# Performance work log

Measured on AMD Instinct MI355X. Metric: run time of the kernel, lower is better.

The kernel has to match this reference:

```python
import jax, jax.numpy as jnp
import numpy as np

N = 2048   # transform dimensionality n
M = 2048   # number of Householder reflectors m (== n -> full expressiveness)
B = 4096   # batch size
H1 = 1.0   # constant for U[-1,-1] when n == m


def setup_inputs() -> dict:
    key = jax.random.key(0)
    k1, k2 = jax.random.split(key)
    x = jax.random.normal(k1, (B, N), dtype=jnp.float32)
    weight = jax.random.normal(k2, (N, M), dtype=jnp.float32)
    return {"x": x, "weight": weight}


def _apply_reflections(x, weight):
    # U = weight.triu(); U[-1,-1] = h1 since n == m
    U = jnp.triu(weight)
    U = U.at[-1, -1].set(jnp.asarray(H1, weight.dtype))
    h = x.T  # (n, B)

    def step(h, u):
        # h <- h - (2 / ||u||^2) * u (u^T h); skip if u == 0 (matches n2==0 branch)
        n2sq = jnp.dot(u, u)
        safe = jnp.where(n2sq > 0, n2sq, jnp.ones_like(n2sq))
        coef = jnp.where(n2sq > 0, 2.0 / safe, jnp.zeros_like(n2sq))
        proj = u @ h  # (B,)
        return h - coef * u[:, None] * proj[None, :], None

    # forward loop runs i = m-1 .. 0, i.e. over reversed rows of U
    h, _ = jax.lax.scan(step, h, U[::-1])
    return h.T  # (B, n)


def reference(x, weight):
    return _apply_reflections(x, weight)
```

## Files before the change

### kernel.cpp

```cpp
#include <hip/hip_runtime.h>


#define NT 2048
#define NT128 16
#define LSTR 48

typedef __attribute__((ext_vector_type(8))) short bf16x8;
typedef __attribute__((ext_vector_type(4))) float f32x4;
typedef unsigned short ushort_t;

__device__ __forceinline__ ushort_t f2bf_rtne(float f) {
  unsigned u = __builtin_bit_cast(unsigned, f);
  u += 0x7FFFu + ((u >> 16) & 1u);
  return (ushort_t)(u >> 16);
}
__device__ __forceinline__ float bf2f(ushort_t h) {
  return __builtin_bit_cast(float, (unsigned)h << 16);
}


__global__ __launch_bounds__(256)
void prep_zero_kernel(const float* __restrict__ w,
                      ushort_t* __restrict__ UMh, ushort_t* __restrict__ UMl,
                      float* __restrict__ Tz) {
  const int b = blockIdx.x;
  if (b >= 4096) {
    const size_t base = ((size_t)(b - 4096) * 256 + threadIdx.x) * 16;
    const float4 z = make_float4(0.f, 0.f, 0.f, 0.f);
#pragma unroll
    for (int q = 0; q < 4; ++q) *(float4*)(Tz + base + q * 4) = z;
    return;
  }
  const size_t i4 = ((size_t)b * 256 + threadIdx.x) * 4;
  const int j = (int)(i4 >> 11);
  const int c = (int)(i4 & (NT - 1));
  const float4 v = *(const float4*)(w + i4);
  float f[4] = {v.x, v.y, v.z, v.w};
  ushort_t h[4], l[4];
#pragma unroll
  for (int q = 0; q < 4; ++q) {
    const int cc = c + q;
    float val = f[q];
    if (j == NT - 1 && cc == NT - 1) val = 1.0f;
    val = (cc >= j) ? val : 0.f;
    h[q] = f2bf_rtne(val);
    l[q] = f2bf_rtne(val - bf2f(h[q]));
  }
  *(uint2*)(UMh + i4) = make_uint2((unsigned)h[0] | ((unsigned)h[1] << 16),
                                   (unsigned)h[2] | ((unsigned)h[3] << 16));
  *(uint2*)(UMl + i4) = make_uint2((unsigned)l[0] | ((unsigned)l[1] << 16),
                                   (unsigned)l[2] | ((unsigned)l[3] << 16));
}


__device__ __forceinline__ void stage_f32ld(const float* __restrict__ src,
                                            int rb, int kb, int t, int ld,
                                            ushort_t* __restrict__ Hd,
                                            ushort_t* __restrict__ Ld) {
  const int r0 = t >> 3;
  const int seg = (t & 7) * 4;
#pragma unroll
  for (int p = 0; p < 4; ++p) {
    const int row = r0 + p * 32;
    const float4 v = *(const float4*)(src + (size_t)(rb + row) * ld + kb + seg);
    const float f[4] = {v.x, v.y, v.z, v.w};
    ushort_t h[4], l[4];
#pragma unroll
    for (int q = 0; q < 4; ++q) {
      h[q] = f2bf_rtne(f[q]);
      l[q] = f2bf_rtne(f[q] - bf2f(h[q]));
    }
    const int o = row * LSTR + seg;
    *(uint2*)(Hd + o) = make_uint2((unsigned)h[0] | ((unsigned)h[1] << 16),
                                   (unsigned)h[2] | ((unsigned)h[3] << 16));
    *(uint2*)(Ld + o) = make_uint2((unsigned)l[0] | ((unsigned)l[1] << 16),
                                   (unsigned)l[2] | ((unsigned)l[3] << 16));
  }
}

__device__ __forceinline__ void stage_a2(const float* __restrict__ A0,
                                         const float* __restrict__ A1,
                                         int rb, int kb, int t, int ld,
                                         ushort_t* __restrict__ Hd,
                                         ushort_t* __restrict__ Ld) {
  const int r0 = t >> 3;
  const int seg = (t & 7) * 4;
#pragma unroll
  for (int p = 0; p < 4; ++p) {
    const int row = r0 + p * 32;
    const size_t g = (size_t)(rb + row) * ld + kb + seg;
    const float4 v0 = *(const float4*)(A0 + g);
    const float4 v1 = *(const float4*)(A1 + g);
    const float f[4] = {v0.x + v1.x, v0.y + v1.y, v0.z + v1.z, v0.w + v1.w};
    ushort_t h[4], l[4];
#pragma unroll
    for (int q = 0; q < 4; ++q) {
      h[q] = f2bf_rtne(f[q]);
      l[q] = f2bf_rtne(f[q] - bf2f(h[q]));
    }
    const int o = row * LSTR + seg;
    *(uint2*)(Hd + o) = make_uint2((unsigned)h[0] | ((unsigned)h[1] << 16),
                                   (unsigned)h[2] | ((unsigned)h[3] << 16));
    *(uint2*)(Ld + o) = make_uint2((unsigned)l[0] | ((unsigned)l[1] << 16),
                                   (unsigned)l[2] | ((unsigned)l[3] << 16));
  }
}

__device__ __forceinline__ void stage_pre(const ushort_t* __restrict__ H,
                                          const ushort_t* __restrict__ L,
                                          int rb, int kb, int t,
                                          ushort_t* __restrict__ Hd,
                                          ushort_t* __restrict__ Ld) {
  const int r0 = t >> 1;
  const int seg = (t & 1) << 4;
  const size_t g = (size_t)(rb + r0) * NT + kb + seg;
  const int o = r0 * LSTR + seg;
  *(bf16x8*)(Hd + o) = *(const bf16x8*)(H + g);
  *(bf16x8*)(Hd + o + 8) = *(const bf16x8*)(H + g + 8);
  *(bf16x8*)(Ld + o) = *(const bf16x8*)(L + g);
  *(bf16x8*)(Ld + o + 8) = *(const bf16x8*)(L + g + 8);
}

__device__ __forceinline__ void stage_pre1(const ushort_t* __restrict__ H,
                                           int rb, int kb, int t,
                                           ushort_t* __restrict__ Hd) {
  const int r0 = t >> 1;
  const int seg = (t & 1) << 4;
  const size_t g = (size_t)(rb + r0) * NT + kb + seg;
  const int o = r0 * LSTR + seg;
  *(bf16x8*)(Hd + o) = *(const bf16x8*)(H + g);
  *(bf16x8*)(Hd + o + 8) = *(const bf16x8*)(H + g + 8);
}

__device__ __forceinline__ void stage_umT(const ushort_t* __restrict__ H,
                                          const ushort_t* __restrict__ L,
                                          int cb, int kb, int t,
                                          ushort_t* __restrict__ Hd,
                                          ushort_t* __restrict__ Ld) {
  const int l = t & 31;
  const int grp = t >> 5;
  const size_t g = (size_t)(kb + l) * NT + cb + grp * 16;
  ushort_t hv[16], lv[16];
  *(uint4*)hv = *(const uint4*)(H + g);
  *(uint4*)(hv + 8) = *(const uint4*)(H + g + 8);
  *(uint4*)lv = *(const uint4*)(L + g);
  *(uint4*)(lv + 8) = *(const uint4*)(L + g + 8);
  const int cbl = grp * 16;
#pragma unroll
  for (int e = 0; e < 16; ++e) {
    const int o = (cbl + e) * LSTR + l;
    Hd[o] = hv[e];
    Ld[o] = lv[e];
  }
}

#define MFMA_BLOCK(Ahs, Als, Bhs, Bls)                                          \
  {                                                                             \
    bf16x8 ah[4], al[4], bh[4], bl[4];                                          \
    _Pragma("unroll") for (int fm = 0; fm < 4; ++fm) {                          \
      const int o = (wm * 64 + fm * 16 + lrow) * LSTR + lk * 8;                 \
      ah[fm] = *(const bf16x8*)(Ahs + o);                                       \
      al[fm] = *(const bf16x8*)(Als + o);                                       \
    }                                                                           \
    _Pragma("unroll") for (int fn = 0; fn < 4; ++fn) {                          \
      const int o = (wn * 64 + fn * 16 + lrow) * LSTR + lk * 8;                 \
      bh[fn] = *(const bf16x8*)(Bhs + o);                                       \
      bl[fn] = *(const bf16x8*)(Bls + o);                                       \
    }                                                                           \
    _Pragma("unroll") for (int fm = 0; fm < 4; ++fm)                            \
      _Pragma("unroll") for (int fn = 0; fn < 4; ++fn) {                        \
        acc[fm][fn] = __builtin_amdgcn_mfma_f32_16x16x32_bf16(ah[fm], bh[fn], acc[fm][fn], 0, 0, 0); \
        acc[fm][fn] = __builtin_amdgcn_mfma_f32_16x16x32_bf16(ah[fm], bl[fn], acc[fm][fn], 0, 0, 0); \
        acc[fm][fn] = __builtin_amdgcn_mfma_f32_16x16x32_bf16(al[fm], bh[fn], acc[fm][fn], 0, 0, 0); \
      }                                                                         \
  }

#define MFMA_BLOCK1(Ahs, Bhs)                                                   \
  {                                                                             \
    bf16x8 ah[4], bh[4];                                                        \
    _Pragma("unroll") for (int fm = 0; fm < 4; ++fm) {                          \
      const int o = (wm * 64 + fm * 16 + lrow) * LSTR + lk * 8;                 \
      ah[fm] = *(const bf16x8*)(Ahs + o);                                       \
    }                                                                           \
    _Pragma("unroll") for (int fn = 0; fn < 4; ++fn) {                          \
      const int o = (wn * 64 + fn * 16 + lrow) * LSTR + lk * 8;                 \
      bh[fn] = *(const bf16x8*)(Bhs + o);                                       \
    }                                                                           \
    _Pragma("unroll") for (int fm = 0; fm < 4; ++fm)                            \
      _Pragma("unroll") for (int fn = 0; fn < 4; ++fn)                          \
        acc[fm][fn] = __builtin_amdgcn_mfma_f32_16x16x32_bf16(ah[fm], bh[fn], acc[fm][fn], 0, 0, 0); \
  }

#define MFMA_DECLS                                                              \
  const int t = threadIdx.x;                                                    \
  const int l = t & 63, w = t >> 6;                                             \
  const int wm = w >> 1, wn = w & 1;                                            \
  const int lrow = l & 15, lk = l >> 4;                                         \
  f32x4 acc[4][4];                                                              \
  _Pragma("unroll") for (int i = 0; i < 4; ++i)                                 \
    _Pragma("unroll") for (int j = 0; j < 4; ++j) {                             \
      acc[i][j][0] = 0.f; acc[i][j][1] = 0.f;                                   \
      acc[i][j][2] = 0.f; acc[i][j][3] = 0.f;                                   \
    }                                                                           \
  (void)l;


__global__ __launch_bounds__(256)
void gram_sk_kernel(const ushort_t* __restrict__ UMh, const ushort_t* __restrict__ UMl,
                    float* __restrict__ Pg) {
  const int b = blockIdx.x;
  const int tile = b / 3, s = b % 3;
  int rem = tile, ti = 0;
  while (rem >= NT128 - ti) { rem -= NT128 - ti; ++ti; }
  const int tj = ti + rem;
  const int mb = ti * 128, nb = tj * 128;
  const int K = NT - nb;
  const int clen = ((K + 2) / 3 + 31) & ~31;
  int cbeg = nb + s * clen, cend = cbeg + clen;
  if (cbeg > NT) cbeg = NT;
  if (cend > NT) cend = NT;

  __shared__ ushort_t Ahs[128 * LSTR], Als[128 * LSTR], Bhs[128 * LSTR], Bls[128 * LSTR];
  MFMA_DECLS

  for (int kb = cbeg; kb < cend; kb += 32) {
    __syncthreads();
    stage_pre(UMh, UMl, mb, kb, t, Ahs, Als);
    stage_pre(UMh, UMl, nb, kb, t, Bhs, Bls);
    __syncthreads();
    MFMA_BLOCK(Ahs, Als, Bhs, Bls)
  }

  float* outp = Pg + (size_t)b * 16384;
#pragma unroll
  for (int fm = 0; fm < 4; ++fm) {
    const int rl = wm * 64 + fm * 16 + lk * 4;
#pragma unroll
    for (int fn = 0; fn < 4; ++fn) {
      const int cl = wn * 64 + fn * 16 + lrow;
#pragma unroll
      for (int r = 0; r < 4; ++r)
        outp[(rl + r) * 128 + cl] = acc[fm][fn][r];
    }
  }
}


__global__ __launch_bounds__(256)
void gred_tbase_kernel(const float* __restrict__ Pg, float* __restrict__ S,
                       float* __restrict__ T, float* __restrict__ Tt) {
  const int b = blockIdx.x;
  if (b < 2176) {
    const size_t idx4 = ((size_t)b * 256 + threadIdx.x) * 4;
    const int tile = (int)(idx4 >> 14);
    const int off = (int)(idx4 & 16383);
    int rem = tile, ti = 0;
    while (rem >= NT128 - ti) { rem -= NT128 - ti; ++ti; }
    const int tj = ti + rem;
    const float* p = Pg + (size_t)tile * 3 * 16384 + off;
    float4 a = *(const float4*)p;
    const float4 b2 = *(const float4*)(p + 16384);
    const float4 c2 = *(const float4*)(p + 32768);
    a.x += b2.x + c2.x; a.y += b2.y + c2.y; a.z += b2.z + c2.z; a.w += b2.w + c2.w;
    *(float4*)(S + (size_t)(ti * 128 + off / 128) * NT + tj * 128 + (off & 127)) = a;
    return;
  }
  __shared__ float Tl[64][65];
  __shared__ float Sb[64][65];
  __shared__ float Z[64][65];
  const int g = b - 2176;
  const int g0 = g * 64;
  const int ti = g >> 1;
  const int roff = (g & 1) * 64;
  const int tidx = 16 * ti - (ti * (ti - 1)) / 2;
  const float* pg = Pg + (size_t)tidx * 3 * 16384;
  const int tt = threadIdx.x;
#pragma unroll
  for (int q = 0; q < 16; ++q) {
    const int e = tt * 16 + q;
    const int i = e >> 6, cc = e & 63;
    const int off = (roff + i) * 128 + roff + cc;
    Sb[i][cc] = pg[off] + pg[16384 + off] + pg[32768 + off];
    Z[i][cc] = 0.f;
  }
  __syncthreads();

  const int zr = tt & 63;
  const int zo = tt >> 6;
  for (int j = 0; j < 64; ++j) {
    if (tt < 64) {
      const float sjj = Sb[j][j];
      const float bj = (sjj > 0.f) ? 2.0f / sjj : 0.f;
      float val;
      if (tt == j) val = bj;
      else if (tt < j) val = -bj * Z[tt][j];
      else val = 0.f;
      Tl[tt][j] = val;
    }
    __syncthreads();
    const float tv = Tl[zr][j];
    if (tv != 0.f) {
      for (int jf = j + 1 + zo; jf < 64; jf += 4)
        Z[zr][jf] = fmaf(tv, Sb[j][jf], Z[zr][jf]);
    }
    __syncthreads();
  }
  if (tt < 64) {
    for (int c = 0; c < 64; ++c) T[(size_t)(g0 + tt) * NT + g0 + c] = Tl[tt][c];
    for (int c = 0; c < 64; ++c) Tt[(size_t)(g0 + c) * NT + g0 + tt] = Tl[tt][c];
  }
}


__device__ __forceinline__
void core64(const float* __restrict__ A, int lda,
            const float* __restrict__ B, int ldb,
            int K, float (&acc)[4][4]) {
  __shared__ float As[16][68];
  __shared__ float Bs[16][68];
  const int tid = threadIdx.x;
  const int tn = tid & 15, tm = tid >> 4;
  const int rowl = tid >> 2;
  const int kq = (tid & 3) << 2;

  for (int c = 0; c < K; c += 16) {
    {
      const float4 v = *(const float4*)(A + (size_t)rowl * lda + c + kq);
      As[kq + 0][rowl] = v.x; As[kq + 1][rowl] = v.y;
      As[kq + 2][rowl] = v.z; As[kq + 3][rowl] = v.w;
      const float4 u = *(const float4*)(B + (size_t)rowl * ldb + c + kq);
      Bs[kq + 0][rowl] = u.x; Bs[kq + 1][rowl] = u.y;
      Bs[kq + 2][rowl] = u.z; Bs[kq + 3][rowl] = u.w;
    }
    __syncthreads();
#pragma unroll
    for (int kk = 0; kk < 16; ++kk) {
      const float4 a4 = *(const float4*)&As[kk][tm * 4];
      const float4 b4 = *(const float4*)&Bs[kk][tn * 4];
      acc[0][0] = fmaf(a4.x, b4.x, acc[0][0]);
      acc[0][1] = fmaf(a4.x, b4.y, acc[0][1]);
      acc[0][2] = fmaf(a4.x, b4.z, acc[0][2]);
      acc[0][3] = fmaf(a4.x, b4.w, acc[0][3]);
      acc[1][0] = fmaf(a4.y, b4.x, acc[1][0]);
      acc[1][1] = fmaf(a4.y, b4.y, acc[1][1]);
      acc[1][2] = fmaf(a4.y, b4.z, acc[1][2]);
      acc[1][3] = fmaf(a4.y, b4.w, acc[1][3]);
      acc[2][0] = fmaf(a4.z, b4.x, acc[2][0]);
      acc[2][1] = fmaf(a4.z, b4.y, acc[2][1]);
      acc[2][2] = fmaf(a4.z, b4.z, acc[2][2]);
      acc[2][3] = fmaf(a4.z, b4.w, acc[2][3]);
      acc[3][0] = fmaf(a4.w, b4.x, acc[3][0]);
      acc[3][1] = fmaf(a4.w, b4.y, acc[3][1]);
      acc[3][2] = fmaf(a4.w, b4.z, acc[3][2]);
      acc[3][3] = fmaf(a4.w, b4.w, acc[3][3]);
    }
    __syncthreads();
  }
}

__global__ __launch_bounds__(256)
void tmerge1_kernel(const float* __restrict__ Tt, const float* __restrict__ S,
                    float* __restrict__ Scv, int k) {
  const int tpk = k >> 6;
  const int tiles = tpk * tpk;
  const int m = blockIdx.x / tiles;
  const int rest = blockIdx.x % tiles;
  const int mb = (rest / tpk) * 64;
  const int nb = (rest % tpk) * 64;
  const int a0 = 2 * k * m, b0 = a0 + k;
  float acc[4][4] = {};
  core64(Tt + (size_t)(b0 + mb) * NT + b0, NT,
         S + (size_t)(a0 + nb) * NT + b0, NT, mb + 64, acc);
  const int tn = threadIdx.x & 15, tm = threadIdx.x >> 4;
#pragma unroll
  for (int i = 0; i < 4; ++i)
#pragma unroll
    for (int jj = 0; jj < 4; ++jj)
      Scv[(size_t)(1024 + mb + tm * 4 + i) * NT + (size_t)m * k + nb + tn * 4 + jj] = acc[i][jj];
}

__global__ __launch_bounds__(256)
void tmerge2_kernel(const float* __restrict__ Scv, float* __restrict__ T,
                    float* __restrict__ Tt, int k) {
  const int tpk = k >> 6;
  const int tiles = tpk * tpk;
  const int m = blockIdx.x / tiles;
  const int rest = blockIdx.x % tiles;
  const int mb = (rest / tpk) * 64;
  const int nb = (rest % tpk) * 64;
  const int a0 = 2 * k * m, b0 = a0 + k;
  float acc[4][4] = {};
  core64(Scv + (size_t)(1024 + mb) * NT + (size_t)m * k + nb, NT,
         T + (size_t)(a0 + nb) * NT + a0 + nb, NT, k - nb, acc);
  const int tn = threadIdx.x & 15, tm = threadIdx.x >> 4;
#pragma unroll
  for (int i = 0; i < 4; ++i) {
    const int q = mb + tm * 4 + i;
#pragma unroll
    for (int jj = 0; jj < 4; ++jj) {
      const int r = nb + tn * 4 + jj;
      const float v = -acc[i][jj];
      Tt[(size_t)(b0 + q) * NT + a0 + r] = v;
      T[(size_t)(a0 + r) * NT + b0 + q] = v;
    }
  }
}

__global__ __launch_bounds__(256)
void tmerge1m_sk(const float* __restrict__ Tt, const float* __restrict__ S,
                 float* __restrict__ P0, float* __restrict__ P1, int k) {
  const int tpk = k >> 7;
  const int tiles = tpk * tpk;
  const int per = tiles * 2;
  const int m = blockIdx.x / per;
  int rest = blockIdx.x % per;
  const int s = rest / tiles; rest %= tiles;
  const int mb = (rest / tpk) * 128;
  const int nb = (rest % tpk) * 128;
  const int a0 = 2 * k * m, b0 = a0 + k;
  const int kend = mb + 128;
  const int half = ((kend >> 1) + 31) & ~31;
  const int kb0 = s ? half : 0;
  const int kb1 = s ? kend : half;

  __shared__ ushort_t Ahs[128 * LSTR], Als[128 * LSTR], Bhs[128 * LSTR], Bls[128 * LSTR];
  MFMA_DECLS

  for (int kb = kb0; kb < kb1; kb += 32) {
    __syncthreads();
    stage_f32ld(Tt + (size_t)b0 * NT + b0, mb, kb, t, NT, Ahs, Als);
    stage_f32ld(S + (size_t)a0 * NT + b0, nb, kb, t, NT, Bhs, Bls);
    __syncthreads();
    MFMA_BLOCK(Ahs, Als, Bhs, Bls)
  }

  float* outp = s ? P1 : P0;
#pragma unroll
  for (int fm = 0; fm < 4; ++fm) {
    const int m0 = mb + wm * 64 + fm * 16 + lk * 4;
#pragma unroll
    for (int fn = 0; fn < 4; ++fn) {
      const int n = nb + wn * 64 + fn * 16 + lrow;
#pragma unroll
      for (int r = 0; r < 4; ++r)
        outp[(size_t)(m0 + r) * NT + (size_t)m * k + n] = acc[fm][fn][r];
    }
  }
}

__global__ __launch_bounds__(256)
void tmerge2m_full(const float* __restrict__ P0, const float* __restrict__ P1,
                   float* __restrict__ T, float* __restrict__ Tt, int k) {
  const int tpk = k >> 7;
  const int tiles = tpk * tpk;
  const int m = blockIdx.x / tiles;
  const int rest = blockIdx.x % tiles;
  const int mb = (rest / tpk) * 128;
  const int nb = (rest % tpk) * 128;
  const int a0 = 2 * k * m, b0 = a0 + k;

  __shared__ ushort_t Ahs[128 * LSTR], Als[128 * LSTR], Bhs[128 * LSTR], Bls[128 * LSTR];
  MFMA_DECLS

  for (int kb = nb; kb < k; kb += 32) {
    __syncthreads();
    stage_a2(P0 + (size_t)m * k, P1 + (size_t)m * k, mb, kb, t, NT, Ahs, Als);
    stage_f32ld(T + (size_t)a0 * NT + a0, nb, kb, t, NT, Bhs, Bls);
    __syncthreads();
    MFMA_BLOCK(Ahs, Als, Bhs, Bls)
  }

#pragma unroll
  for (int fm = 0; fm < 4; ++fm) {
    const int q0 = mb + wm * 64 + fm * 16 + lk * 4;
#pragma unroll
    for (int fn = 0; fn < 4; ++fn) {
      const int r = nb + wn * 64 + fn * 16 + lrow;
#pragma unroll
      for (int e = 0; e < 4; ++e) {
        const float v = -acc[fm][fn][e];
        Tt[(size_t)(b0 + q0 + e) * NT + a0 + r] = v;
        T[(size_t)(a0 + r) * NT + b0 + q0 + e] = v;
      }
    }
  }
}

__global__ __launch_bounds__(256)
void tmerge2m_sk(const float* __restrict__ P0, const float* __restrict__ P1,
                 const float* __restrict__ T, float* __restrict__ Pq, int k) {
  const int tpk = k >> 7;
  const int tiles = tpk * tpk;
  int rest = blockIdx.x % (tiles * 2);
  const int s = rest / tiles; rest %= tiles;
  const int tile = rest;
  const int mb = (rest / tpk) * 128;
  const int nb = (rest % tpk) * 128;
  const int len = k - nb;
  const int half = ((len >> 1) + 31) & ~31;
  const int kb0 = nb + (s ? half : 0);
  const int kb1 = s ? k : nb + half;

  __shared__ ushort_t Ahs[128 * LSTR], Als[128 * LSTR], Bhs[128 * LSTR], Bls[128 * LSTR];
  MFMA_DECLS

  for (int kb = kb0; kb < kb1; kb += 32) {
    __syncthreads();
    stage_a2(P0, P1, mb, kb, t, NT, Ahs, Als);
    stage_f32ld(T, nb, kb, t, NT, Bhs, Bls);
    __syncthreads();
    MFMA_BLOCK(Ahs, Als, Bhs, Bls)
  }

  float* outp = Pq + (size_t)(tile * 2 + s) * 16384;
#pragma unroll
  for (int fm = 0; fm < 4; ++fm) {
    const int rl = wm * 64 + fm * 16 + lk * 4;
#pragma unroll
    for (int fn = 0; fn < 4; ++fn) {
      const int cl = wn * 64 + fn * 16 + lrow;
#pragma unroll
      for (int r = 0; r < 4; ++r)
        outp[(rl + r) * 128 + cl] = acc[fm][fn][r];
    }
  }
}

__global__ __launch_bounds__(256)
void t2reduce_kernel(const float* __restrict__ Pq, float* __restrict__ T,
                     float* __restrict__ Tt) {
  const size_t idx4 = ((size_t)blockIdx.x * 256 + threadIdx.x) * 4;
  const int tile = (int)(idx4 >> 14);
  const int off = (int)(idx4 & 16383);
  const int ti2 = tile / 8, tj2 = tile % 8;
  const int q = ti2 * 128 + off / 128;
  const int r = tj2 * 128 + (off & 127);
  const float* p = Pq + (size_t)tile * 2 * 16384 + off;
  const float4 a = *(const float4*)p;
  const float4 b2 = *(const float4*)(p + 16384);
  float4 v;
  v.x = -(a.x + b2.x); v.y = -(a.y + b2.y);
  v.z = -(a.z + b2.z); v.w = -(a.w + b2.w);
  *(float4*)(Tt + (size_t)(1024 + q) * NT + r) = v;
}


__global__ __launch_bounds__(256)
void wbuild_sk(const ushort_t* __restrict__ UMh, const ushort_t* __restrict__ UMl,
               const float* __restrict__ Tt, float* __restrict__ Pw) {
  const int b = blockIdx.x;
  int tile, s;
  if (b < 256) { tile = b; s = 0; }
  else { const int bb = b - 256; tile = ((bb / 9) + 7) * 16 + (bb % 9) + 7; s = 1; }
  const int ti = tile >> 4, tj = tile & 15;
  const int mb = ti * 128, nb = tj * 128;
  const int kend = ((mb < nb ? mb : nb)) + 128;
  const int big = (ti >= 7 && tj >= 7);
  const int half = big ? (kend >> 1) : kend;
  const int kb0 = s ? half : 0;
  const int kb1 = s ? kend : half;

  __shared__ ushort_t Ahs[128 * LSTR], Als[128 * LSTR], Bhs[128 * LSTR], Bls[128 * LSTR];
  MFMA_DECLS

  for (int kb = kb0; kb < kb1; kb += 32) {
    __syncthreads();
    stage_umT(UMh, UMl, mb, kb, t, Ahs, Als);
    stage_f32ld(Tt, nb, kb, t, NT, Bhs, Bls);
    __syncthreads();
    MFMA_BLOCK(Ahs, Als, Bhs, Bls)
  }

  float* outp = Pw + (size_t)b * 16384;
#pragma unroll
  for (int fm = 0; fm < 4; ++fm) {
    const int rl = wm * 64 + fm * 16 + lk * 4;
#pragma unroll
    for (int fn = 0; fn < 4; ++fn) {
      const int cl = wn * 64 + fn * 16 + lrow;
#pragma unroll
      for (int r = 0; r < 4; ++r)
        outp[(rl + r) * 128 + cl] = acc[fm][fn][r];
    }
  }
}

__global__ __launch_bounds__(256)
void wreduce_kernel(const float* __restrict__ Pw,
                    ushort_t* __restrict__ Wh, ushort_t* __restrict__ Wl) {
  const size_t idx4 = ((size_t)blockIdx.x * 256 + threadIdx.x) * 4;
  const int tile = (int)(idx4 >> 14);
  const int off = (int)(idx4 & 16383);
  const int ti = tile >> 4, tj = tile & 15;
  float4 a = *(const float4*)(Pw + (size_t)tile * 16384 + off);
  if (ti >= 7 && tj >= 7) {
    const int slot = 256 + (ti - 7) * 9 + (tj - 7);
    const float4 b2 = *(const float4*)(Pw + (size_t)slot * 16384 + off);
    a.x += b2.x; a.y += b2.y; a.z += b2.z; a.w += b2.w;
  }
  const float f[4] = {a.x, a.y, a.z, a.w};
  ushort_t h[4], l[4];
#pragma unroll
  for (int e = 0; e < 4; ++e) {
    h[e] = f2bf_rtne(f[e]);
    l[e] = f2bf_rtne(f[e] - bf2f(h[e]));
  }
  const size_t o = (size_t)(ti * 128 + off / 128) * NT + tj * 128 + (off & 127);
  *(uint2*)(Wh + o) = make_uint2((unsigned)h[0] | ((unsigned)h[1] << 16),
                                 (unsigned)h[2] | ((unsigned)h[3] << 16));
  *(uint2*)(Wl + o) = make_uint2((unsigned)l[0] | ((unsigned)l[1] << 16),
                                 (unsigned)l[2] | ((unsigned)l[3] << 16));
}


__global__ __launch_bounds__(256)
void q2build_sk(const ushort_t* __restrict__ Wh, const ushort_t* __restrict__ Wl,
                const ushort_t* __restrict__ UMh, const ushort_t* __restrict__ UMl,
                ushort_t* __restrict__ Q2h, ushort_t* __restrict__ Q2l,
                float* __restrict__ Pp) {
  const int b = blockIdx.x;
  int ti, nb_t, s, SK, slot;
  if (b < 128) {
    ti = b >> 3; nb_t = b & 7; s = 0; SK = 1; slot = -1;
  } else if (b < 320) {
    const int idx = b - 128;
    const int tile = idx / 3; s = idx % 3;
    ti = tile >> 2; nb_t = 8 + (tile & 3); SK = 3;
    slot = tile * 3 + s;
  } else {
    const int idx = b - 320;
    const int tile = idx / 4; s = idx % 4;
    ti = tile >> 2; nb_t = 12 + (tile & 3); SK = 4;
    slot = 192 + tile * 4 + s;
  }
  const int mb = ti * 128, nb = nb_t * 128;
  const int kend = nb + 128;
  int kb0, kb1;
  if (SK == 1) {
    kb0 = 0; kb1 = kend;
  } else {
    const int step = (((kend + SK - 1) / SK) + 31) & ~31;
    kb0 = s * step;
    kb1 = kb0 + step;
    if (kb1 > kend) kb1 = kend;
    if (kb0 > kend) kb0 = kend;
  }

  __shared__ ushort_t Ahs[128 * LSTR], Als[128 * LSTR], Bhs[128 * LSTR], Bls[128 * LSTR];
  MFMA_DECLS

  for (int kb = kb0; kb < kb1; kb += 32) {
    __syncthreads();
    stage_pre(Wh, Wl, mb, kb, t, Ahs, Als);
    stage_umT(UMh, UMl, nb, kb, t, Bhs, Bls);
    __syncthreads();
    MFMA_BLOCK(Ahs, Als, Bhs, Bls)
  }

  if (SK == 1) {
#pragma unroll
    for (int fm = 0; fm < 4; ++fm) {
      const int d0 = mb + wm * 64 + fm * 16 + lk * 4;
#pragma unroll
      for (int fn = 0; fn < 4; ++fn) {
        const int c = nb + wn * 64 + fn * 16 + lrow;
#pragma unroll
        for (int r = 0; r < 4; ++r) {
          const int d = d0 + r;
          const float f = ((d == c) ? 1.0f : 0.0f) - acc[fm][fn][r];
          const size_t idx = (size_t)d * NT + c;
          const ushort_t h = f2bf_rtne(f);
          Q2h[idx] = h;
          Q2l[idx] = f2bf_rtne(f - bf2f(h));
        }
      }
    }
  } else {
    float* outp = Pp + (size_t)slot * 16384;
#pragma unroll
    for (int fm = 0; fm < 4; ++fm) {
      const int rl = wm * 64 + fm * 16 + lk * 4;
#pragma unroll
      for (int fn = 0; fn < 4; ++fn) {
        const int cl = wn * 64 + fn * 16 + lrow;
#pragma unroll
        for (int r = 0; r < 4; ++r)
          outp[(rl + r) * 128 + cl] = acc[fm][fn][r];
      }
    }
  }
}


__global__ __launch_bounds__(256)
void q2red_prepx_kernel(const float* __restrict__ Pp,
                        ushort_t* __restrict__ Q2h, ushort_t* __restrict__ Q2l,
                        const float* __restrict__ x,
                        ushort_t* __restrict__ Xh, ushort_t* __restrict__ Xl) {
  const int b = blockIdx.x;
  if (b < 2048) {
    const size_t idx4 = ((size_t)b * 256 + threadIdx.x) * 4;
    const int tile = (int)(idx4 >> 14);
    const int off = (int)(idx4 & 16383);
    int ti, nb_t, base, SK;
    if (tile < 64) {
      ti = tile >> 2; nb_t = 8 + (tile & 3); base = tile * 3; SK = 3;
    } else {
      const int pb = tile - 64;
      ti = pb >> 2; nb_t = 12 + (pb & 3); base = 192 + pb * 4; SK = 4;
    }
    const float* p = Pp + (size_t)base * 16384 + off;
    float sum[4] = {0.f, 0.f, 0.f, 0.f};
    for (int sl = 0; sl < SK; ++sl) {
      const float4 v = *(const float4*)(p + (size_t)sl * 16384);
      sum[0] += v.x; sum[1] += v.y; sum[2] += v.z; sum[3] += v.w;
    }
    const int d = ti * 128 + off / 128;
    const int c0 = nb_t * 128 + (off & 127);
    ushort_t h[4], l[4];
#pragma unroll
    for (int e = 0; e < 4; ++e) {
      const float f = ((d == c0 + e) ? 1.0f : 0.0f) - sum[e];
      h[e] = f2bf_rtne(f);
      l[e] = f2bf_rtne(f - bf2f(h[e]));
    }
    const size_t o = (size_t)d * NT + c0;
    *(uint2*)(Q2h + o) = make_uint2((unsigned)h[0] | ((unsigned)h[1] << 16),
                                    (unsigned)h[2] | ((unsigned)h[3] << 16));
    *(uint2*)(Q2l + o) = make_uint2((unsigned)l[0] | ((unsigned)l[1] << 16),
                                    (unsigned)l[2] | ((unsigned)l[3] << 16));
    return;
  }
  const size_t i4 = (((size_t)(b - 2048)) * 256 + threadIdx.x) * 4;
  const float4 v = *(const float4*)(x + i4);
  const float f[4] = {v.x, v.y, v.z, v.w};
  ushort_t h[4], l[4];
#pragma unroll
  for (int q = 0; q < 4; ++q) {
    h[q] = f2bf_rtne(f[q]);
    l[q] = f2bf_rtne(f[q] - bf2f(h[q]));
  }
  *(uint2*)(Xh + i4) = make_uint2((unsigned)h[0] | ((unsigned)h[1] << 16),
                                  (unsigned)h[2] | ((unsigned)h[3] << 16));
  *(uint2*)(Xl + i4) = make_uint2((unsigned)l[0] | ((unsigned)l[1] << 16),
                                  (unsigned)l[2] | ((unsigned)l[3] << 16));
}


__global__ __launch_bounds__(256)
void gemm_app_kernel(const ushort_t* __restrict__ Xh, const ushort_t* __restrict__ Xl,
                     const ushort_t* __restrict__ Q2h, const ushort_t* __restrict__ Q2l,
                     float* __restrict__ Cf) {
  __shared__ ushort_t Ahs[128 * LSTR], Bhs[128 * LSTR];
  int bid = blockIdx.x;
  const int nwg = gridDim.x;
  if ((nwg & 7) == 0) {
    const int q = nwg >> 3;
    bid = (bid & 7) * q + (bid >> 3);
  }
  const int mb = (bid / NT128) * 128;
  const int nb = (bid % NT128) * 128;
  (void)Xl; (void)Q2l;

  MFMA_DECLS

  for (int kb = 0; kb < NT; kb += 32) {
    __syncthreads();
    stage_pre1(Xh, mb, kb, t, Ahs);
    stage_pre1(Q2h, nb, kb, t, Bhs);
    __syncthreads();
    MFMA_BLOCK1(Ahs, Bhs)
  }

#pragma unroll
  for (int fm = 0; fm < 4; ++fm) {
    const int m0 = mb + wm * 64 + fm * 16 + lk * 4;
#pragma unroll
    for (int fn = 0; fn < 4; ++fn) {
      const int n = nb + wn * 64 + fn * 16 + lrow;
#pragma unroll
      for (int r = 0; r < 4; ++r)
        Cf[(size_t)(m0 + r) * NT + n] = acc[fm][fn][r];
    }
  }
}


#define NRF 32
#define VCF 2
#define KGF 8
#define WPBF 4
#define NGRAMF ((KGF * (KGF + 1)) / 2)
#define NREDF (NGRAMF + KGF * VCF)

__device__ __forceinline__ void accum_group_f(const float (&u)[KGF],
                                              const float (&hr)[VCF],
                                              float (&red)[NREDF]) {
#pragma unroll
  for (int j = 0; j < KGF; ++j) {
#pragma unroll
    for (int l = 0; l <= j; ++l)
      red[(j * (j + 1)) / 2 + l] = fmaf(u[j], u[l], red[(j * (j + 1)) / 2 + l]);
#pragma unroll
    for (int c = 0; c < VCF; ++c)
      red[NGRAMF + j * VCF + c] = fmaf(u[j], hr[c], red[NGRAMF + j * VCF + c]);
  }
}

__global__ __launch_bounds__(256, 2)
void fallback_sweep_kernel(const float* __restrict__ x,
                           const float* __restrict__ w,
                           float* __restrict__ out) {
  const int lane = threadIdx.x & 63;
  const int wave = threadIdx.x >> 6;
  const int gw = blockIdx.x * WPBF + wave;
  const int col0 = gw * VCF;
  float h[NRF][VCF];
#pragma unroll
  for (int k = 0; k < NRF; ++k) {
    const int r = lane + 64 * k;
#pragma unroll
    for (int c = 0; c < VCF; ++c) h[k][c] = x[(size_t)(col0 + c) * NT + r];
  }
  for (int i0 = NT - KGF; i0 >= 0; i0 -= KGF) {
    const int ks = i0 >> 6;
    const float* wb = w + (size_t)i0 * NT;
    float red[NREDF];
#pragma unroll
    for (int t = 0; t < NREDF; ++t) red[t] = 0.f;
#pragma unroll
    for (int k = 0; k < NRF; ++k) {
      const int r = lane + 64 * k;
      if (k > ks) {
        float u[KGF];
#pragma unroll
        for (int j = 0; j < KGF; ++j) u[j] = wb[(size_t)j * NT + r];
        accum_group_f(u, h[k], red);
      } else if (k == ks) {
        float u[KGF];
#pragma unroll
        for (int j = 0; j < KGF; ++j) {
          float tt = wb[(size_t)j * NT + r];
          u[j] = (r >= i0 + j) ? tt : 0.f;
        }
        if (i0 == NT - KGF && r == NT - 1) u[KGF - 1] = 1.0f;
        accum_group_f(u, h[k], red);
      }
    }
#pragma unroll
    for (int m = 1; m < 64; m <<= 1)
#pragma unroll
      for (int t = 0; t < NREDF; ++t) red[t] += __shfl_xor(red[t], m, 64);
    float beta[KGF];
#pragma unroll
    for (int j = 0; j < KGF; ++j) {
      const float n2 = red[(j * (j + 1)) / 2 + j];
      beta[j] = (n2 > 0.f) ? 2.0f / n2 : 0.f;
    }
    float T[KGF][KGF];
#pragma unroll
    for (int j = 0; j < KGF; ++j) {
      T[j][j] = beta[j];
#pragma unroll
      for (int r0 = 0; r0 < j; ++r0) {
        float acc = 0.f;
#pragma unroll
        for (int l = r0; l < j; ++l)
          acc = fmaf(T[r0][l], red[(j * (j + 1)) / 2 + l], acc);
        T[r0][j] = -beta[j] * acc;
      }
    }
    float z[KGF][VCF];
#pragma unroll
    for (int j = 0; j < KGF; ++j)
#pragma unroll
      for (int c = 0; c < VCF; ++c) {
        float acc = 0.f;
#pragma unroll
        for (int l = j; l < KGF; ++l)
          acc = fmaf(T[j][l], red[NGRAMF + l * VCF + c], acc);
        z[j][c] = acc;
      }
#pragma unroll
    for (int k = 0; k < NRF; ++k) {
      const int r = lane + 64 * k;
      if (k >= ks) {
        float u[KGF];
#pragma unroll
        for (int j = 0; j < KGF; ++j) {
          float tt = wb[(size_t)j * NT + r];
          u[j] = (k > ks || r >= i0 + j) ? tt : 0.f;
        }
        if (i0 == NT - KGF && r == NT - 1) u[KGF - 1] = 1.0f;
#pragma unroll
        for (int c = 0; c < VCF; ++c) {
          float acc = h[k][c];
#pragma unroll
          for (int j = 0; j < KGF; ++j) acc = fmaf(-u[j], z[j][c], acc);
          h[k][c] = acc;
        }
      }
    }
  }
#pragma unroll
  for (int k = 0; k < NRF; ++k) {
    const int r = lane + 64 * k;
#pragma unroll
    for (int c = 0; c < VCF; ++c)
      out[(size_t)(col0 + c) * NT + r] = h[k][c];
  }
}


extern "C" void kernel_launch(void* const* d_in, const int* in_sizes, int n_in,
                              void* d_out, int out_size, void* d_ws, size_t ws_size,
                              hipStream_t stream) {
  const float* x = (const float*)d_in[0];
  const float* w = (const float*)d_in[1];
  float* out = (float*)d_out;
  const int Bsz = in_sizes[0] / NT;

  const size_t NW = (size_t)NT * NT;
  float* ws = (float*)d_ws;

  float* S  = ws;
  float* T  = ws + NW;
  float* Tt = ws + 2 * NW;
  ushort_t* UMh = (ushort_t*)(ws + 3 * NW);
  ushort_t* UMl = UMh + NW;
  ushort_t* Wh = (ushort_t*)ws;
  ushort_t* Wl = (ushort_t*)(ws + NW / 2);
  ushort_t* Q2h = (ushort_t*)(ws + NW);
  ushort_t* Q2l = (ushort_t*)(ws + 3 * NW / 2);
  ushort_t* Xh = (ushort_t*)(ws + 3 * NW);
  ushort_t* Xl = Xh + (size_t)Bsz * NT;
  float* scratch = (float*)d_out;

  const size_t need = 4 * NW * sizeof(float);

  if (ws_size < need || (Bsz % 128) != 0 || out_size < (int)(2 * NW)) {
    fallback_sweep_kernel<<<Bsz / (VCF * WPBF), 256, 0, stream>>>(x, w, out);
    return;
  }

  prep_zero_kernel<<<4096 + 2048, 256, 0, stream>>>(w, UMh, UMl, T);

  gram_sk_kernel<<<136 * 3, 256, 0, stream>>>(UMh, UMl, scratch);

  gred_tbase_kernel<<<2176 + 32, 256, 0, stream>>>(scratch, S, T, Tt);

  for (int k = 64; k <= 256; k <<= 1) {
    const int mm = NT / (2 * k);
    const int grid = mm * (k >> 6) * (k >> 6);
    tmerge1_kernel<<<grid, 256, 0, stream>>>(Tt, S, S, k);
    tmerge2_kernel<<<grid, 256, 0, stream>>>(S, T, Tt, k);
  }
  {
    const int k = 512, mm = 2, tiles = 16;
    float* P0 = S + (size_t)1024 * NT;
    float* P1 = S + (size_t)1536 * NT;
    tmerge1m_sk<<<mm * tiles * 2, 256, 0, stream>>>(Tt, S, P0, P1, k);
    tmerge2m_full<<<mm * tiles, 256, 0, stream>>>(P0, P1, T, Tt, k);
  }
  {
    const int k = 1024, tiles = 64;
    float* P0 = S + (size_t)1024 * NT;
    float* P1 = T + (size_t)1024 * NT;
    tmerge1m_sk<<<tiles * 2, 256, 0, stream>>>(Tt, S, P0, P1, k);
    tmerge2m_sk<<<tiles * 2, 256, 0, stream>>>(P0, P1, T, scratch, k);
    t2reduce_kernel<<<(64 * 16384) / 1024, 256, 0, stream>>>(scratch, T, Tt);
  }

  wbuild_sk<<<337, 256, 0, stream>>>(UMh, UMl, Tt, scratch);
  wreduce_kernel<<<(256 * 16384) / 1024, 256, 0, stream>>>(scratch, Wh, Wl);

  q2build_sk<<<576, 256, 0, stream>>>(Wh, Wl, UMh, UMl, Q2h, Q2l, scratch);

  q2red_prepx_kernel<<<2048 + (int)((size_t)Bsz * NT / 1024), 256, 0, stream>>>(
      scratch, Q2h, Q2l, x, Xh, Xl);

  const int grid = (Bsz / 128) * NT128;
  gemm_app_kernel<<<grid, 256, 0, stream>>>(Xh, Xl, Q2h, Q2l, out);
}
```

Baseline: 462.1 us.

## Pre-transpose UM for vectorized staging and drop unused low-part writes

```diff
diff --git a/kernel.cpp b/kernel.cpp
--- a/kernel.cpp
+++ b/kernel.cpp
@@ -50,6 +50,34 @@
                                    (unsigned)h[2] | ((unsigned)h[3] << 16));
   *(uint2*)(UMl + i4) = make_uint2((unsigned)l[0] | ((unsigned)l[1] << 16),
                                    (unsigned)l[2] | ((unsigned)l[3] << 16));
+}
+
+
+__global__ __launch_bounds__(256)
+void trans_um_kernel(const ushort_t* __restrict__ UMh, const ushort_t* __restrict__ UMl,
+                     ushort_t* __restrict__ UMTh, ushort_t* __restrict__ UMTl) {
+  __shared__ ushort_t Th[64][80], Tl2[64][80];
+  const int bj = (blockIdx.x & 31) * 64;
+  const int bc = (blockIdx.x >> 5) * 64;
+  const int r = threadIdx.x >> 2;
+  const int s = (threadIdx.x & 3) * 16;
+  const size_t g = (size_t)(bj + r) * NT + bc + s;
+  *(uint4*)&Th[r][s] = *(const uint4*)(UMh + g);
+  *(uint4*)&Th[r][s + 8] = *(const uint4*)(UMh + g + 8);
+  *(uint4*)&Tl2[r][s] = *(const uint4*)(UMl + g);
+  *(uint4*)&Tl2[r][s + 8] = *(const uint4*)(UMl + g + 8);
+  __syncthreads();
+  ushort_t oh[16], ol[16];
+#pragma unroll
+  for (int e = 0; e < 16; ++e) {
+    oh[e] = Th[s + e][r];
+    ol[e] = Tl2[s + e][r];
+  }
+  const size_t o = (size_t)(bc + r) * NT + bj + s;
+  *(uint4*)(UMTh + o) = *(uint4*)oh;
+  *(uint4*)(UMTh + o + 8) = *(uint4*)(oh + 8);
+  *(uint4*)(UMTl + o) = *(uint4*)ol;
+  *(uint4*)(UMTl + o + 8) = *(uint4*)(ol + 8);
 }
 
 
@@ -130,28 +158,6 @@
   const int o = r0 * LSTR + seg;
   *(bf16x8*)(Hd + o) = *(const bf16x8*)(H + g);
   *(bf16x8*)(Hd + o + 8) = *(const bf16x8*)(H + g + 8);
-}
-
-__device__ __forceinline__ void stage_umT(const ushort_t* __restrict__ H,
-                                          const ushort_t* __restrict__ L,
-                                          int cb, int kb, int t,
-                                          ushort_t* __restrict__ Hd,
-                                          ushort_t* __restrict__ Ld) {
-  const int l = t & 31;
-  const int grp = t >> 5;
-  const size_t g = (size_t)(kb + l) * NT + cb + grp * 16;
-  ushort_t hv[16], lv[16];
-  *(uint4*)hv = *(const uint4*)(H + g);
-  *(uint4*)(hv + 8) = *(const uint4*)(H + g + 8);
-  *(uint4*)lv = *(const uint4*)(L + g);
-  *(uint4*)(lv + 8) = *(const uint4*)(L + g + 8);
-  const int cbl = grp * 16;
-#pragma unroll
-  for (int e = 0; e < 16; ++e) {
-    const int o = (cbl + e) * LSTR + l;
-    Hd[o] = hv[e];
-    Ld[o] = lv[e];
-  }
 }
 
 #define MFMA_BLOCK(Ahs, Als, Bhs, Bls)                                          \
@@ -546,7 +552,7 @@
 
 
 __global__ __launch_bounds__(256)
-void wbuild_sk(const ushort_t* __restrict__ UMh, const ushort_t* __restrict__ UMl,
+void wbuild_sk(const ushort_t* __restrict__ UMTh, const ushort_t* __restrict__ UMTl,
                const float* __restrict__ Tt, float* __restrict__ Pw) {
   const int b = blockIdx.x;
   int tile, s;
@@ -565,7 +571,7 @@
 
   for (int kb = kb0; kb < kb1; kb += 32) {
     __syncthreads();
-    stage_umT(UMh, UMl, mb, kb, t, Ahs, Als);
+    stage_pre(UMTh, UMTl, mb, kb, t, Ahs, Als);
     stage_f32ld(Tt, nb, kb, t, NT, Bhs, Bls);
     __syncthreads();
     MFMA_BLOCK(Ahs, Als, Bhs, Bls)
@@ -615,36 +621,18 @@
 
 __global__ __launch_bounds__(256)
 void q2build_sk(const ushort_t* __restrict__ Wh, const ushort_t* __restrict__ Wl,
-                const ushort_t* __restrict__ UMh, const ushort_t* __restrict__ UMl,
-                ushort_t* __restrict__ Q2h, ushort_t* __restrict__ Q2l,
-                float* __restrict__ Pp) {
+                const ushort_t* __restrict__ UMTh, const ushort_t* __restrict__ UMTl,
+                ushort_t* __restrict__ Q2h, float* __restrict__ Pp) {
   const int b = blockIdx.x;
-  int ti, nb_t, s, SK, slot;
-  if (b < 128) {
-    ti = b >> 3; nb_t = b & 7; s = 0; SK = 1; slot = -1;
-  } else if (b < 320) {
-    const int idx = b - 128;
-    const int tile = idx / 3; s = idx % 3;
-    ti = tile >> 2; nb_t = 8 + (tile & 3); SK = 3;
-    slot = tile * 3 + s;
-  } else {
-    const int idx = b - 320;
-    const int tile = idx / 4; s = idx % 4;
-    ti = tile >> 2; nb_t = 12 + (tile & 3); SK = 4;
-    slot = 192 + tile * 4 + s;
-  }
+  int ti, nb_t, s;
+  if (b < 256) { ti = b >> 4; nb_t = b & 15; s = 0; }
+  else { const int bb = b - 256; ti = bb >> 3; nb_t = 8 + (bb & 7); s = 1; }
   const int mb = ti * 128, nb = nb_t * 128;
   const int kend = nb + 128;
-  int kb0, kb1;
-  if (SK == 1) {
-    kb0 = 0; kb1 = kend;
-  } else {
-    const int step = (((kend + SK - 1) / SK) + 31) & ~31;
-    kb0 = s * step;
-    kb1 = kb0 + step;
-    if (kb1 > kend) kb1 = kend;
-    if (kb0 > kend) kb0 = kend;
-  }
+  const int split = (nb_t >= 8);
+  const int half = split ? (kend >> 1) : kend;
+  const int kb0 = s ? half : 0;
+  const int kb1 = s ? kend : half;
 
   __shared__ ushort_t Ahs[128 * LSTR], Als[128 * LSTR], Bhs[128 * LSTR], Bls[128 * LSTR];
   MFMA_DECLS
@@ -652,12 +640,12 @@
   for (int kb = kb0; kb < kb1; kb += 32) {
     __syncthreads();
     stage_pre(Wh, Wl, mb, kb, t, Ahs, Als);
-    stage_umT(UMh, UMl, nb, kb, t, Bhs, Bls);
+    stage_pre(UMTh, UMTl, nb, kb, t, Bhs, Bls);
     __syncthreads();
     MFMA_BLOCK(Ahs, Als, Bhs, Bls)
   }
 
-  if (SK == 1) {
+  if (!split) {
 #pragma unroll
     for (int fm = 0; fm < 4; ++fm) {
       const int d0 = mb + wm * 64 + fm * 16 + lk * 4;
@@ -668,15 +656,12 @@
         for (int r = 0; r < 4; ++r) {
           const int d = d0 + r;
           const float f = ((d == c) ? 1.0f : 0.0f) - acc[fm][fn][r];
-          const size_t idx = (size_t)d * NT + c;
-          const ushort_t h = f2bf_rtne(f);
-          Q2h[idx] = h;
-          Q2l[idx] = f2bf_rtne(f - bf2f(h));
+          Q2h[(size_t)d * NT + c] = f2bf_rtne(f);
         }
       }
     }
   } else {
-    float* outp = Pp + (size_t)slot * 16384;
+    float* outp = Pp + (size_t)((ti * 8 + (nb_t - 8)) * 2 + s) * 16384;
 #pragma unroll
     for (int fm = 0; fm < 4; ++fm) {
       const int rl = wm * 64 + fm * 16 + lk * 4;
@@ -694,62 +679,46 @@
 
 __global__ __launch_bounds__(256)
 void q2red_prepx_kernel(const float* __restrict__ Pp,
-                        ushort_t* __restrict__ Q2h, ushort_t* __restrict__ Q2l,
+                        ushort_t* __restrict__ Q2h,
                         const float* __restrict__ x,
-                        ushort_t* __restrict__ Xh, ushort_t* __restrict__ Xl) {
+                        ushort_t* __restrict__ Xh) {
   const int b = blockIdx.x;
   if (b < 2048) {
     const size_t idx4 = ((size_t)b * 256 + threadIdx.x) * 4;
     const int tile = (int)(idx4 >> 14);
     const int off = (int)(idx4 & 16383);
-    int ti, nb_t, base, SK;
-    if (tile < 64) {
-      ti = tile >> 2; nb_t = 8 + (tile & 3); base = tile * 3; SK = 3;
-    } else {
-      const int pb = tile - 64;
-      ti = pb >> 2; nb_t = 12 + (pb & 3); base = 192 + pb * 4; SK = 4;
-    }
-    const float* p = Pp + (size_t)base * 16384 + off;
-    float sum[4] = {0.f, 0.f, 0.f, 0.f};
-    for (int sl = 0; sl < SK; ++sl) {
-      const float4 v = *(const float4*)(p + (size_t)sl * 16384);
-      sum[0] += v.x; sum[1] += v.y; sum[2] += v.z; sum[3] += v.w;
-    }
+    const int ti = tile >> 3, nbb = tile & 7;
+    const float* p = Pp + (size_t)tile * 2 * 16384 + off;
+    const float4 a = *(const float4*)p;
+    const float4 b2 = *(const float4*)(p + 16384);
     const int d = ti * 128 + off / 128;
-    const int c0 = nb_t * 128 + (off & 127);
-    ushort_t h[4], l[4];
+    const int c0 = (8 + nbb) * 128 + (off & 127);
+    const float sum[4] = {a.x + b2.x, a.y + b2.y, a.z + b2.z, a.w + b2.w};
+    ushort_t h[4];
 #pragma unroll
     for (int e = 0; e < 4; ++e) {
       const float f = ((d == c0 + e) ? 1.0f : 0.0f) - sum[e];
       h[e] = f2bf_rtne(f);
-      l[e] = f2bf_rtne(f - bf2f(h[e]));
-    }
-    const size_t o = (size_t)d * NT + c0;
-    *(uint2*)(Q2h + o) = make_uint2((unsigned)h[0] | ((unsigned)h[1] << 16),
-                                    (unsigned)h[2] | ((unsigned)h[3] << 16));
-    *(uint2*)(Q2l + o) = make_uint2((unsigned)l[0] | ((unsigned)l[1] << 16),
-                                    (unsigned)l[2] | ((unsigned)l[3] << 16));
+    }
+    *(uint2*)(Q2h + (size_t)d * NT + c0) =
+        make_uint2((unsigned)h[0] | ((unsigned)h[1] << 16),
+                   (unsigned)h[2] | ((unsigned)h[3] << 16));
     return;
   }
   const size_t i4 = (((size_t)(b - 2048)) * 256 + threadIdx.x) * 4;
   const float4 v = *(const float4*)(x + i4);
   const float f[4] = {v.x, v.y, v.z, v.w};
-  ushort_t h[4], l[4];
-#pragma unroll
-  for (int q = 0; q < 4; ++q) {
-    h[q] = f2bf_rtne(f[q]);
-    l[q] = f2bf_rtne(f[q] - bf2f(h[q]));
-  }
+  ushort_t h[4];
+#pragma unroll
+  for (int q = 0; q < 4; ++q) h[q] = f2bf_rtne(f[q]);
   *(uint2*)(Xh + i4) = make_uint2((unsigned)h[0] | ((unsigned)h[1] << 16),
                                   (unsigned)h[2] | ((unsigned)h[3] << 16));
-  *(uint2*)(Xl + i4) = make_uint2((unsigned)l[0] | ((unsigned)l[1] << 16),
-                                  (unsigned)l[2] | ((unsigned)l[3] << 16));
-}
-
-
-__global__ __launch_bounds__(256)
-void gemm_app_kernel(const ushort_t* __restrict__ Xh, const ushort_t* __restrict__ Xl,
-                     const ushort_t* __restrict__ Q2h, const ushort_t* __restrict__ Q2l,
+}
+
+
+__global__ __launch_bounds__(256)
+void gemm_app_kernel(const ushort_t* __restrict__ Xh,
+                     const ushort_t* __restrict__ Q2h,
                      float* __restrict__ Cf) {
   __shared__ ushort_t Ahs[128 * LSTR], Bhs[128 * LSTR];
   int bid = blockIdx.x;
@@ -760,7 +729,6 @@
   }
   const int mb = (bid / NT128) * 128;
   const int nb = (bid % NT128) * 128;
-  (void)Xl; (void)Q2l;
 
   MFMA_DECLS
 
@@ -922,6 +890,7 @@
 
   const size_t NW = (size_t)NT * NT;
   float* ws = (float*)d_ws;
+  float* scratch = (float*)d_out;
 
   float* S  = ws;
   float* T  = ws + NW;
@@ -931,10 +900,9 @@
   ushort_t* Wh = (ushort_t*)ws;
   ushort_t* Wl = (ushort_t*)(ws + NW / 2);
   ushort_t* Q2h = (ushort_t*)(ws + NW);
-  ushort_t* Q2l = (ushort_t*)(ws + 3 * NW / 2);
+  ushort_t* UMTh = (ushort_t*)(ws + NW + NW / 2);
+  ushort_t* UMTl = (ushort_t*)(scratch + NW + NW / 2);
   ushort_t* Xh = (ushort_t*)(ws + 3 * NW);
-  ushort_t* Xl = Xh + (size_t)Bsz * NT;
-  float* scratch = (float*)d_out;
 
   const size_t need = 4 * NW * sizeof(float);
 
@@ -971,14 +939,16 @@
     t2reduce_kernel<<<(64 * 16384) / 1024, 256, 0, stream>>>(scratch, T, Tt);
   }
 
-  wbuild_sk<<<337, 256, 0, stream>>>(UMh, UMl, Tt, scratch);
+  trans_um_kernel<<<1024, 256, 0, stream>>>(UMh, UMl, UMTh, UMTl);
+
+  wbuild_sk<<<337, 256, 0, stream>>>(UMTh, UMTl, Tt, scratch);
   wreduce_kernel<<<(256 * 16384) / 1024, 256, 0, stream>>>(scratch, Wh, Wl);
 
-  q2build_sk<<<576, 256, 0, stream>>>(Wh, Wl, UMh, UMl, Q2h, Q2l, scratch);
+  q2build_sk<<<384, 256, 0, stream>>>(Wh, Wl, UMTh, UMTl, Q2h, scratch);
 
   q2red_prepx_kernel<<<2048 + (int)((size_t)Bsz * NT / 1024), 256, 0, stream>>>(
-      scratch, Q2h, Q2l, x, Xh, Xl);
+      scratch, Q2h, x, Xh);
 
   const int grid = (Bsz / 128) * NT128;
-  gemm_app_kernel<<<grid, 256, 0, stream>>>(Xh, Xl, Q2h, Q2l, out);
-}
+  gemm_app_kernel<<<grid, 256, 0, stream>>>(Xh, Q2h, out);
+}
```

After: 455.5 us. Within noise of the previous version (-1.4%).
